# Performance work log

Hardware: AMD Instinct MI355X
Metric: run time of the kernel (lower is better)

## Reference

```python
import jax, jax.numpy as jnp
import numpy as np

N, n, D1, D2 = 16, 1024, 64, 64


def setup_inputs() -> dict:
    key = jax.random.key(0)
    ks = jax.random.split(key, 17)
    f = lambda k, shape: jax.random.normal(k, shape, dtype=jnp.float32)
    return {
        "A": f(ks[0], (N, n, n)),
        "X": f(ks[1], (N, n, D1)),
        "coeffs": f(ks[2], (5,)),
        "wA1": f(ks[3], (1, D1)),
        "wA2": f(ks[4], (1, D1)),
        "w11": f(ks[5], (D2, D1)),
        "w12": f(ks[6], (D2, D1)),
        "w13": f(ks[7], (D2, 1)),
        "w14": f(ks[8], (D2, 1)),
        "w15": f(ks[9], (D2, 1)),
        "w16": f(ks[10], (D2, 1)),
        "w21": f(ks[11], (D2, D1)),
        "w22": f(ks[12], (D2, D1)),
        "w23": f(ks[13], (D2, 1)),
        "w24": f(ks[14], (D2, 1)),
        "w25": f(ks[15], (D2, 1)),
        "w26": f(ks[16], (D2, 1)),
    }


def reference(A, X, coeffs, wA1, wA2, w11, w12, w13, w14, w15, w16,
              w21, w22, w23, w24, w25, w26):
    nn_ = A.shape[-1]
    diag = jnp.diagonal(A, axis1=-2, axis2=-1)          # (N, n)
    mean_diag = diag.mean(-1)                            # (N,)
    rowmean = A.mean(-1)                                 # (N, n) mean over columns
    mean_all = rowmean.mean(-1)                          # (N,)
    mean_X = X.mean(1)                                   # (N, D1)

    p1 = X @ wA1[0]                                      # (N, n)   Linear(D1->1) per node
    p2 = mean_X @ wA2[0]                                 # (N,)     Linear(D1->1) on mean

    # adjacency transform: scalar-weighted A + scalar stats + symmetrized row stats
    A_t = (coeffs[0] * A
           + (coeffs[1] * mean_all + coeffs[2] * mean_diag + p2)[:, None, None]
           + coeffs[3] * (rowmean[:, None, :] + rowmean[:, :, None])
           + coeffs[4] * (diag[:, None, :] + diag[:, :, None])
           + p1[:, None, :] + p1[:, :, None])             # (N, n, n)

    def node_transform(w_x, w_mx, w_col, w_diag, w_mdiag, w_mall):
        per_graph = (mean_X @ w_mx.T                      # (N, D2)
                     + mean_diag[:, None] * w_mdiag[:, 0][None, :]
                     + mean_all[:, None] * w_mall[:, 0][None, :])
        return (jnp.einsum('bnd,ed->bne', X, w_x)         # (N, n, D2)
                + rowmean[:, :, None] * w_col[:, 0]
                + diag[:, :, None] * w_diag[:, 0]
                + per_graph[:, None, :])

    X1_t = node_transform(w11, w12, w13, w14, w15, w16)
    X2_t = node_transform(w21, w22, w23, w24, w25, w26)

    out = A_t @ X2_t / nn_ + X1_t                         # (N, n, D2)
    return (A_t, out)
```

## Files before the change

### kernel.cpp

```cpp
#include <hip/hip_runtime.h>
#include <hip/hip_bf16.h>

#define NGRAPH 16
#define NNODE 1024
#define DDIM 64

typedef __attribute__((ext_vector_type(8))) short bf16x8;
typedef __attribute__((ext_vector_type(4))) float f32x4;

#define OFF_ROWSUM 0
#define OFF_DIAG   16384
#define OFF_P1     32768
#define OFF_R      49152
#define OFF_CS     65536
#define OFF_S      73728
#define OFF_S2P    75840
#define OFF_R2P    92224
#define OFF_BASE0  110656
#define OFF_X2T    1159232

__device__ __forceinline__ unsigned short f2bf(float f) {
    unsigned int u = __float_as_uint(f);
    u = (u + 0x7fffu + ((u >> 16) & 1u)) >> 16;
    return (unsigned short)u;
}

__device__ __forceinline__ unsigned int cvt_pk_bf16(float lo, float hi) {
    unsigned int r;
    asm("v_cvt_pk_bf16_f32 %0, %1, %2" : "=v"(r) : "v"(lo), "v"(hi));
    return r;
}

__device__ __forceinline__ float wave_reduce(float v) {
    #pragma unroll
    for (int off = 32; off; off >>= 1) v += __shfl_down(v, off, 64);
    return v;
}

__global__ __launch_bounds__(256) void kA_stats(const float* __restrict__ A,
                                                const float* __restrict__ X,
                                                const float* __restrict__ wA1,
                                                float* __restrict__ rowsum,
                                                float* __restrict__ diagv,
                                                float* __restrict__ p1,
                                                float* __restrict__ colsum_part) {
    if (blockIdx.x < NGRAPH * NNODE / 4) {
        int row  = blockIdx.x * 4 + (threadIdx.x >> 6);
        int lane = threadIdx.x & 63;
        const float4* b4 = (const float4*)(A + (size_t)row * NNODE);
        float sum = 0.f;
        #pragma unroll
        for (int it = 0; it < 4; ++it) {
            float4 v = b4[lane + it * 64];
            sum += v.x + v.y + v.z + v.w;
        }
        sum = wave_reduce(sum);
        if (lane == 0) {
            rowsum[row] = sum;
            int i = row & (NNODE - 1);
            diagv[row] = ((const float*)b4)[i];
        }
    } else {
        int bid  = blockIdx.x - NGRAPH * NNODE / 4;
        int b    = bid >> 3;
        int blk  = bid & 7;
        int wv   = threadIdx.x >> 6;
        int lane = threadIdx.x & 63;
        float w = wA1[lane];
        float cs = 0.f;
        int row0 = blk * 128 + wv * 32;
        const float* Xb = X + (size_t)b * NNODE * DDIM;
        for (int rI = 0; rI < 32; ++rI) {
            int i = row0 + rI;
            float x = Xb[i * DDIM + lane];
            cs += x;
            float v = wave_reduce(x * w);
            if (lane == 0) p1[b * NNODE + i] = v;
        }
        __shared__ float csl[4][64];
        csl[wv][lane] = cs;
        __syncthreads();
        if (threadIdx.x < 64) {
            float t = csl[0][lane] + csl[1][lane] + csl[2][lane] + csl[3][lane];
            colsum_part[(b * 8 + blk) * 64 + lane] = t;
        }
    }
}

__global__ __launch_bounds__(256) void kB_nodes(const float* __restrict__ X,
                                                const float* __restrict__ coeffs,
                                                const float* __restrict__ wA2,
                                                const float* __restrict__ w11,
                                                const float* __restrict__ w12,
                                                const float* __restrict__ w13,
                                                const float* __restrict__ w14,
                                                const float* __restrict__ w15,
                                                const float* __restrict__ w16,
                                                const float* __restrict__ w21,
                                                const float* __restrict__ w22,
                                                const float* __restrict__ w23,
                                                const float* __restrict__ w24,
                                                const float* __restrict__ w25,
                                                const float* __restrict__ w26,
                                                const float* __restrict__ rowsum,
                                                const float* __restrict__ diagv,
                                                const float* __restrict__ colsum_part,
                                                const float* __restrict__ p1g,
                                                float* __restrict__ rws,
                                                float* __restrict__ base0,
                                                unsigned short* __restrict__ x2tg,
                                                float* __restrict__ S2part,
                                                float* __restrict__ R2part,
                                                float* __restrict__ sArr) {
    __shared__ float Xl[64][68];
    __shared__ float w1l[64][68];
    __shared__ float w2l[64][68];
    __shared__ unsigned short X2Tl[64][68];
    __shared__ float rm_l[64], dg_l[64], r_l[64];
    __shared__ float redS[4][64], redR[4][64];
    __shared__ float redA[4], redD[4];
    __shared__ float mxs[64], p2s;
    __shared__ float pg1_l[64], pg2_l[64];

    int b    = blockIdx.x >> 4;
    int tile = blockIdx.x & 15;
    int i0   = tile * 64;
    int tid  = threadIdx.x;
    int e    = tid & 63;
    int wv   = tid >> 6;

    const float* Xg = X + (size_t)b * (NNODE * DDIM) + (size_t)i0 * DDIM;
    #pragma unroll
    for (int it = 0; it < 4; ++it) {
        int g   = it * 256 + tid;
        int row = g >> 4;
        int c4  = (g & 15) << 2;
        float4 v  = ((const float4*)Xg)[g];
        *(float4*)&Xl[row][c4] = v;
        float4 v1 = ((const float4*)w11)[g];
        *(float4*)&w1l[row][c4] = v1;
        float4 v2 = ((const float4*)w21)[g];
        *(float4*)&w2l[row][c4] = v2;
    }

    float sa = 0.f, sd = 0.f;
    for (int i = tid; i < NNODE; i += 256) {
        sa += rowsum[b * NNODE + i];
        sd += diagv[b * NNODE + i];
    }
    sa = wave_reduce(sa); sd = wave_reduce(sd);
    if (e == 0) { redA[wv] = sa; redD[wv] = sd; }
    if (tid < 64) {
        float mx = 0.f;
        for (int k = 0; k < 8; ++k) mx += colsum_part[(b * 8 + k) * 64 + tid];
        mxs[tid] = mx * (1.f / (float)NNODE);
    }
    __syncthreads();
    float mean_all  = (redA[0] + redA[1] + redA[2] + redA[3]) * (1.f / ((float)NNODE * (float)NNODE));
    float mean_diag = (redD[0] + redD[1] + redD[2] + redD[3]) * (1.f / (float)NNODE);
    float c3 = coeffs[3], c4c = coeffs[4];

    if (wv == 0) {
        float a1 = 0.f;
        for (int d = 0; d < 64; ++d) a1 += mxs[d] * w12[e * 64 + d];
        pg1_l[e] = a1 + mean_diag * w15[e] + mean_all * w16[e];
    } else if (wv == 1) {
        float a2 = 0.f;
        for (int d = 0; d < 64; ++d) a2 += mxs[d] * w22[e * 64 + d];
        pg2_l[e] = a2 + mean_diag * w25[e] + mean_all * w26[e];
    } else if (wv == 2) {
        float v = wave_reduce(mxs[e] * wA2[e]);
        if (e == 0) p2s = v;
    } else {
        float rs  = rowsum[b * NNODE + i0 + e];
        float dgv = diagv[b * NNODE + i0 + e];
        float rmv = rs * (1.f / (float)NNODE);
        rm_l[e] = rmv;
        dg_l[e] = dgv;
        float rv = c3 * rmv + c4c * dgv + p1g[b * NNODE + i0 + e];
        r_l[e] = rv;
        rws[b * NNODE + i0 + e] = rv;
    }
    __syncthreads();
    if (tile == 0 && tid == 0)
        sArr[b] = coeffs[1] * mean_all + coeffs[2] * mean_diag + p2s;

    float w13e = w13[e], w14e = w14[e], w23e = w23[e], w24e = w24[e];
    float pg1e = pg1_l[e], pg2e = pg2_l[e];

    float acc1[16], acc2[16];
    #pragma unroll
    for (int t = 0; t < 16; ++t) { acc1[t] = 0.f; acc2[t] = 0.f; }

    for (int d0 = 0; d0 < 64; d0 += 4) {
        float4 w1v = *(const float4*)&w1l[e][d0];
        float4 w2v = *(const float4*)&w2l[e][d0];
        #pragma unroll
        for (int t = 0; t < 16; ++t) {
            int li = wv + 4 * t;
            float4 xv = *(const float4*)&Xl[li][d0];
            acc1[t] += xv.x * w1v.x + xv.y * w1v.y + xv.z * w1v.z + xv.w * w1v.w;
            acc2[t] += xv.x * w2v.x + xv.y * w2v.y + xv.z * w2v.z + xv.w * w2v.w;
        }
    }

    float s2acc = 0.f, r2acc = 0.f;
    #pragma unroll
    for (int t = 0; t < 16; ++t) {
        int li = wv + 4 * t;
        int i  = i0 + li;
        float rmv = rm_l[li], dgv = dg_l[li];
        float x2t = acc2[t] + rmv * w23e + dgv * w24e + pg2e;
        float b0  = acc1[t] + rmv * w13e + dgv * w14e + pg1e;
        base0[((size_t)(b * NNODE + i)) * 64 + e] = b0;
        X2Tl[e][li] = f2bf(x2t);
        s2acc += x2t;
        r2acc += r_l[li] * x2t;
    }
    redS[wv][e] = s2acc;
    redR[wv][e] = r2acc;
    __syncthreads();

    for (int k = 0; k < 16; ++k) {
        int ep = wv * 16 + k;
        unsigned short v = X2Tl[ep][e];
        x2tg[((size_t)(b * 64 + ep)) * NNODE + i0 + e] = v;
    }
    if (tid < 64) {
        float s2 = redS[0][tid] + redS[1][tid] + redS[2][tid] + redS[3][tid];
        float r2 = redR[0][tid] + redR[1][tid] + redR[2][tid] + redR[3][tid];
        S2part[(b * 16 + tile) * 64 + tid] = s2;
        R2part[(b * 16 + tile) * 64 + tid] = r2;
    }
}

__global__ __launch_bounds__(256) void kC_main(const float* __restrict__ A,
                                               const float* __restrict__ coeffs,
                                               const float* __restrict__ sArr,
                                               const float* __restrict__ rArr,
                                               const unsigned short* __restrict__ x2tg,
                                               const float* __restrict__ base0,
                                               const float* __restrict__ S2part,
                                               const float* __restrict__ R2part,
                                               float* __restrict__ At,
                                               float* __restrict__ outp) {
    __shared__ unsigned short Al[2][16][132];
    __shared__ float r_lds[1024];
    __shared__ float s2_lds[64], r2_lds[64];

    int b    = blockIdx.x >> 6;
    int tile = blockIdx.x & 63;
    int i0   = tile * 16;
    int tid  = threadIdx.x;

    float4 rv = ((const float4*)(rArr + b * NNODE))[tid];
    *(float4*)&r_lds[tid * 4] = rv;
    if (tid < 64) {
        float s2 = 0.f, r2 = 0.f;
        #pragma unroll
        for (int t = 0; t < 16; ++t) {
            s2 += S2part[(b * 16 + t) * 64 + tid];
            r2 += R2part[(b * 16 + t) * 64 + tid];
        }
        s2_lds[tid] = s2 * (1.f / (float)NNODE);
        r2_lds[tid] = r2 * (1.f / (float)NNODE);
    }

    float sb  = sArr[b];
    float c0  = coeffs[0];
    float c0n = c0 * (1.f / (float)NNODE);

    int arow = tid >> 4;
    int acol = (tid & 15) * 8;
    const float* Ab  = A  + ((size_t)(b * NNODE + i0 + arow)) * NNODE + acol;
    float*       Atb = At + ((size_t)(b * NNODE + i0 + arow)) * NNODE + acol;

    int lane = tid & 63, wv = tid >> 6;
    int m = lane & 15, quad = lane >> 4;
    int e = wv * 16 + m;
    const unsigned short* Bg = x2tg + ((size_t)(b * 64 + e)) * NNODE + quad * 8;

    float4 a0 = *(const float4*)(Ab);
    float4 a1 = *(const float4*)(Ab + 4);
    bf16x8 bf0 = *(const bf16x8*)(Bg);
    bf16x8 bf1 = *(const bf16x8*)(Bg + 32);
    bf16x8 bf2 = *(const bf16x8*)(Bg + 64);
    bf16x8 bf3 = *(const bf16x8*)(Bg + 96);

    f32x4 acc = {0.f, 0.f, 0.f, 0.f};

    __syncthreads();

    float bse = sb + r_lds[i0 + arow];

    #pragma unroll
    for (int kt = 0; kt < 8; ++kt) {
        int cidx = kt * 128 + acol;
        float4 rj0 = *(const float4*)&r_lds[cidx];
        float4 rj1 = *(const float4*)&r_lds[cidx + 4];
        f32x4 t0, t1;
        t0.x = fmaf(c0, a0.x, bse + rj0.x);
        t0.y = fmaf(c0, a0.y, bse + rj0.y);
        t0.z = fmaf(c0, a0.z, bse + rj0.z);
        t0.w = fmaf(c0, a0.w, bse + rj0.w);
        t1.x = fmaf(c0, a1.x, bse + rj1.x);
        t1.y = fmaf(c0, a1.y, bse + rj1.y);
        t1.z = fmaf(c0, a1.z, bse + rj1.z);
        t1.w = fmaf(c0, a1.w, bse + rj1.w);
        *(f32x4*)(Atb + kt * 128)     = t0;
        *(f32x4*)(Atb + kt * 128 + 4) = t1;

        uint4 pk;
        pk.x = cvt_pk_bf16(a0.x, a0.y);
        pk.y = cvt_pk_bf16(a0.z, a0.w);
        pk.z = cvt_pk_bf16(a1.x, a1.y);
        pk.w = cvt_pk_bf16(a1.z, a1.w);
        *(uint4*)&Al[kt & 1][arow][acol] = pk;

        bf16x8 n0, n1, n2, n3;
        if (kt < 7) {
            a0 = *(const float4*)(Ab + (kt + 1) * 128);
            a1 = *(const float4*)(Ab + (kt + 1) * 128 + 4);
            n0 = *(const bf16x8*)(Bg + (kt + 1) * 128);
            n1 = *(const bf16x8*)(Bg + (kt + 1) * 128 + 32);
            n2 = *(const bf16x8*)(Bg + (kt + 1) * 128 + 64);
            n3 = *(const bf16x8*)(Bg + (kt + 1) * 128 + 96);
        }

        asm volatile("s_waitcnt lgkmcnt(0)\n\ts_barrier" ::: "memory");

        bf16x8 av0 = *(const bf16x8*)&Al[kt & 1][m][quad * 8];
        bf16x8 av1 = *(const bf16x8*)&Al[kt & 1][m][32 + quad * 8];
        bf16x8 av2 = *(const bf16x8*)&Al[kt & 1][m][64 + quad * 8];
        bf16x8 av3 = *(const bf16x8*)&Al[kt & 1][m][96 + quad * 8];
        acc = __builtin_amdgcn_mfma_f32_16x16x32_bf16(av0, bf0, acc, 0, 0, 0);
        acc = __builtin_amdgcn_mfma_f32_16x16x32_bf16(av1, bf1, acc, 0, 0, 0);
        acc = __builtin_amdgcn_mfma_f32_16x16x32_bf16(av2, bf2, acc, 0, 0, 0);
        acc = __builtin_amdgcn_mfma_f32_16x16x32_bf16(av3, bf3, acc, 0, 0, 0);

        if (kt < 7) { bf0 = n0; bf1 = n1; bf2 = n2; bf3 = n3; }
    }

    float s2 = s2_lds[e];
    float r2 = r2_lds[e];
    #pragma unroll
    for (int reg = 0; reg < 4; ++reg) {
        int i = i0 + quad * 4 + reg;
        float v = acc[reg] * c0n
                + base0[((size_t)(b * NNODE + i)) * 64 + e]
                + (sb + r_lds[i]) * s2 + r2;
        outp[((size_t)(b * NNODE + i)) * 64 + e] = v;
    }
}

extern "C" void kernel_launch(void* const* d_in, const int* in_sizes, int n_in,
                              void* d_out, int out_size, void* d_ws, size_t ws_size,
                              hipStream_t stream) {
    const float* A      = (const float*)d_in[0];
    const float* X      = (const float*)d_in[1];
    const float* coeffs = (const float*)d_in[2];
    const float* wA1    = (const float*)d_in[3];
    const float* wA2    = (const float*)d_in[4];
    const float* w11    = (const float*)d_in[5];
    const float* w12    = (const float*)d_in[6];
    const float* w13    = (const float*)d_in[7];
    const float* w14    = (const float*)d_in[8];
    const float* w15    = (const float*)d_in[9];
    const float* w16    = (const float*)d_in[10];
    const float* w21    = (const float*)d_in[11];
    const float* w22    = (const float*)d_in[12];
    const float* w23    = (const float*)d_in[13];
    const float* w24    = (const float*)d_in[14];
    const float* w25    = (const float*)d_in[15];
    const float* w26    = (const float*)d_in[16];

    float* ws  = (float*)d_ws;
    float* At  = (float*)d_out;
    float* out = (float*)d_out + (size_t)NGRAPH * NNODE * NNODE;

    float* rowsum = ws + OFF_ROWSUM;
    float* diagv  = ws + OFF_DIAG;
    float* p1     = ws + OFF_P1;
    float* rws    = ws + OFF_R;
    float* cspart = ws + OFF_CS;
    float* sArr   = ws + OFF_S;
    float* S2part = ws + OFF_S2P;
    float* R2part = ws + OFF_R2P;
    float* base0  = ws + OFF_BASE0;
    unsigned short* x2tg = (unsigned short*)(ws + OFF_X2T);

    kA_stats<<<NGRAPH * NNODE / 4 + NGRAPH * 8, 256, 0, stream>>>(
        A, X, wA1, rowsum, diagv, p1, cspart);
    kB_nodes<<<NGRAPH * 16, 256, 0, stream>>>(
        X, coeffs, wA2, w11, w12, w13, w14, w15, w16,
        w21, w22, w23, w24, w25, w26,
        rowsum, diagv, cspart, p1,
        rws, base0, x2tg, S2part, R2part, sArr);
    kC_main<<<NGRAPH * 64, 256, 0, stream>>>(
        A, coeffs, sArr, rws, x2tg, base0, S2part, R2part, At, out);
}
```

Measured before the change: 205.3 us.

## Give each wave its own 16-row strip and drop LDS staging of A

Each wave now owns a 16-row strip of A and computes all 64 output columns through four accumulators. The A fragment goes straight from registers into MFMA operands, which removes the LDS staging buffer and the per-iteration barrier. The grid shrinks from 1024 to 256 blocks. In exchange, every wave loads the whole x2t B panel itself instead of sharing it across waves, and the larger register footprint with fewer blocks may reduce the latency hiding available for this streaming kernel.

```diff
diff --git a/kernel.cpp b/kernel.cpp
--- a/kernel.cpp
+++ b/kernel.cpp
@@ -244,14 +244,15 @@
                                                const float* __restrict__ R2part,
                                                float* __restrict__ At,
                                                float* __restrict__ outp) {
-    __shared__ unsigned short Al[2][16][132];
     __shared__ float r_lds[1024];
     __shared__ float s2_lds[64], r2_lds[64];
 
-    int b    = blockIdx.x >> 6;
-    int tile = blockIdx.x & 63;
-    int i0   = tile * 16;
+    int b    = blockIdx.x >> 4;
+    int tb   = blockIdx.x & 15;
     int tid  = threadIdx.x;
+    int lane = tid & 63, wv = tid >> 6;
+    int i0   = (tb * 4 + wv) * 16;
+    int m    = lane & 15, q = lane >> 4;
 
     float4 rv = ((const float4*)(rArr + b * NNODE))[tid];
     *(float4*)&r_lds[tid * 4] = rv;
@@ -270,86 +271,97 @@
     float c0  = coeffs[0];
     float c0n = c0 * (1.f / (float)NNODE);
 
-    int arow = tid >> 4;
-    int acol = (tid & 15) * 8;
-    const float* Ab  = A  + ((size_t)(b * NNODE + i0 + arow)) * NNODE + acol;
-    float*       Atb = At + ((size_t)(b * NNODE + i0 + arow)) * NNODE + acol;
-
-    int lane = tid & 63, wv = tid >> 6;
-    int m = lane & 15, quad = lane >> 4;
-    int e = wv * 16 + m;
-    const unsigned short* Bg = x2tg + ((size_t)(b * 64 + e)) * NNODE + quad * 8;
-
-    float4 a0 = *(const float4*)(Ab);
-    float4 a1 = *(const float4*)(Ab + 4);
-    bf16x8 bf0 = *(const bf16x8*)(Bg);
-    bf16x8 bf1 = *(const bf16x8*)(Bg + 32);
-    bf16x8 bf2 = *(const bf16x8*)(Bg + 64);
-    bf16x8 bf3 = *(const bf16x8*)(Bg + 96);
-
-    f32x4 acc = {0.f, 0.f, 0.f, 0.f};
+    const float* Aw  = A  + ((size_t)(b * NNODE + i0 + m)) * NNODE + q * 8;
+    float*       Atw = At + ((size_t)(b * NNODE + i0 + m)) * NNODE + q * 8;
+    const unsigned short* Bw = x2tg + ((size_t)(b * 64 + m)) * NNODE + q * 8;
+
+    f32x4 a[8], an[8];
+    #pragma unroll
+    for (int ks = 0; ks < 4; ++ks) {
+        a[2 * ks]     = *(const f32x4*)(Aw + ks * 32);
+        a[2 * ks + 1] = *(const f32x4*)(Aw + ks * 32 + 4);
+    }
+
+    f32x4 acc[4];
+    #pragma unroll
+    for (int s = 0; s < 4; ++s) acc[s] = (f32x4){0.f, 0.f, 0.f, 0.f};
 
     __syncthreads();
 
-    float bse = sb + r_lds[i0 + arow];
-
-    #pragma unroll
+    float bse = sb + r_lds[i0 + m];
+
+    #pragma unroll 2
     for (int kt = 0; kt < 8; ++kt) {
-        int cidx = kt * 128 + acol;
-        float4 rj0 = *(const float4*)&r_lds[cidx];
-        float4 rj1 = *(const float4*)&r_lds[cidx + 4];
-        f32x4 t0, t1;
-        t0.x = fmaf(c0, a0.x, bse + rj0.x);
-        t0.y = fmaf(c0, a0.y, bse + rj0.y);
-        t0.z = fmaf(c0, a0.z, bse + rj0.z);
-        t0.w = fmaf(c0, a0.w, bse + rj0.w);
-        t1.x = fmaf(c0, a1.x, bse + rj1.x);
-        t1.y = fmaf(c0, a1.y, bse + rj1.y);
-        t1.z = fmaf(c0, a1.z, bse + rj1.z);
-        t1.w = fmaf(c0, a1.w, bse + rj1.w);
-        *(f32x4*)(Atb + kt * 128)     = t0;
-        *(f32x4*)(Atb + kt * 128 + 4) = t1;
-
-        uint4 pk;
-        pk.x = cvt_pk_bf16(a0.x, a0.y);
-        pk.y = cvt_pk_bf16(a0.z, a0.w);
-        pk.z = cvt_pk_bf16(a1.x, a1.y);
-        pk.w = cvt_pk_bf16(a1.z, a1.w);
-        *(uint4*)&Al[kt & 1][arow][acol] = pk;
-
-        bf16x8 n0, n1, n2, n3;
+        bf16x8 Bf[4][4];
+        #pragma unroll
+        for (int s = 0; s < 4; ++s) {
+            #pragma unroll
+            for (int ks = 0; ks < 4; ++ks) {
+                Bf[s][ks] = *(const bf16x8*)(Bw + (size_t)s * 16 * NNODE + kt * 128 + ks * 32);
+            }
+        }
+
         if (kt < 7) {
-            a0 = *(const float4*)(Ab + (kt + 1) * 128);
-            a1 = *(const float4*)(Ab + (kt + 1) * 128 + 4);
-            n0 = *(const bf16x8*)(Bg + (kt + 1) * 128);
-            n1 = *(const bf16x8*)(Bg + (kt + 1) * 128 + 32);
-            n2 = *(const bf16x8*)(Bg + (kt + 1) * 128 + 64);
-            n3 = *(const bf16x8*)(Bg + (kt + 1) * 128 + 96);
-        }
-
-        asm volatile("s_waitcnt lgkmcnt(0)\n\ts_barrier" ::: "memory");
-
-        bf16x8 av0 = *(const bf16x8*)&Al[kt & 1][m][quad * 8];
-        bf16x8 av1 = *(const bf16x8*)&Al[kt & 1][m][32 + quad * 8];
-        bf16x8 av2 = *(const bf16x8*)&Al[kt & 1][m][64 + quad * 8];
-        bf16x8 av3 = *(const bf16x8*)&Al[kt & 1][m][96 + quad * 8];
-        acc = __builtin_amdgcn_mfma_f32_16x16x32_bf16(av0, bf0, acc, 0, 0, 0);
-        acc = __builtin_amdgcn_mfma_f32_16x16x32_bf16(av1, bf1, acc, 0, 0, 0);
-        acc = __builtin_amdgcn_mfma_f32_16x16x32_bf16(av2, bf2, acc, 0, 0, 0);
-        acc = __builtin_amdgcn_mfma_f32_16x16x32_bf16(av3, bf3, acc, 0, 0, 0);
-
-        if (kt < 7) { bf0 = n0; bf1 = n1; bf2 = n2; bf3 = n3; }
-    }
-
-    float s2 = s2_lds[e];
-    float r2 = r2_lds[e];
-    #pragma unroll
-    for (int reg = 0; reg < 4; ++reg) {
-        int i = i0 + quad * 4 + reg;
-        float v = acc[reg] * c0n
-                + base0[((size_t)(b * NNODE + i)) * 64 + e]
-                + (sb + r_lds[i]) * s2 + r2;
-        outp[((size_t)(b * NNODE + i)) * 64 + e] = v;
+            #pragma unroll
+            for (int ks = 0; ks < 4; ++ks) {
+                an[2 * ks]     = *(const f32x4*)(Aw + (kt + 1) * 128 + ks * 32);
+                an[2 * ks + 1] = *(const f32x4*)(Aw + (kt + 1) * 128 + ks * 32 + 4);
+            }
+        }
+
+        bf16x8 pka[4];
+        #pragma unroll
+        for (int ks = 0; ks < 4; ++ks) {
+            int cb = kt * 128 + ks * 32 + q * 8;
+            f32x4 rj0 = *(const f32x4*)&r_lds[cb];
+            f32x4 rj1 = *(const f32x4*)&r_lds[cb + 4];
+            f32x4 ac0 = a[2 * ks], ac1 = a[2 * ks + 1];
+            f32x4 t0, t1;
+            t0.x = fmaf(c0, ac0.x, bse + rj0.x);
+            t0.y = fmaf(c0, ac0.y, bse + rj0.y);
+            t0.z = fmaf(c0, ac0.z, bse + rj0.z);
+            t0.w = fmaf(c0, ac0.w, bse + rj0.w);
+            t1.x = fmaf(c0, ac1.x, bse + rj1.x);
+            t1.y = fmaf(c0, ac1.y, bse + rj1.y);
+            t1.z = fmaf(c0, ac1.z, bse + rj1.z);
+            t1.w = fmaf(c0, ac1.w, bse + rj1.w);
+            *(f32x4*)(Atw + kt * 128 + ks * 32)     = t0;
+            *(f32x4*)(Atw + kt * 128 + ks * 32 + 4) = t1;
+
+            union { uint4 u; bf16x8 h; } cv;
+            cv.u.x = cvt_pk_bf16(ac0.x, ac0.y);
+            cv.u.y = cvt_pk_bf16(ac0.z, ac0.w);
+            cv.u.z = cvt_pk_bf16(ac1.x, ac1.y);
+            cv.u.w = cvt_pk_bf16(ac1.z, ac1.w);
+            pka[ks] = cv.h;
+        }
+
+        #pragma unroll
+        for (int s = 0; s < 4; ++s) {
+            #pragma unroll
+            for (int ks = 0; ks < 4; ++ks) {
+                acc[s] = __builtin_amdgcn_mfma_f32_16x16x32_bf16(pka[ks], Bf[s][ks], acc[s], 0, 0, 0);
+            }
+        }
+
+        if (kt < 7) {
+            #pragma unroll
+            for (int u = 0; u < 8; ++u) a[u] = an[u];
+        }
+    }
+
+    #pragma unroll
+    for (int s = 0; s < 4; ++s) {
+        float s2 = s2_lds[s * 16 + m];
+        float r2 = r2_lds[s * 16 + m];
+        #pragma unroll
+        for (int reg = 0; reg < 4; ++reg) {
+            int i = i0 + q * 4 + reg;
+            float v = acc[s][reg] * c0n
+                    + base0[((size_t)(b * NNODE + i)) * 64 + s * 16 + m]
+                    + (sb + r_lds[i]) * s2 + r2;
+            outp[((size_t)(b * NNODE + i)) * 64 + s * 16 + m] = v;
+        }
     }
 }
 
@@ -396,6 +408,6 @@
         w21, w22, w23, w24, w25, w26,
         rowsum, diagv, cspart, p1,
         rws, base0, x2tg, S2part, R2part, sArr);
-    kC_main<<<NGRAPH * 64, 256, 0, stream>>>(
+    kC_main<<<NGRAPH * 16, 256, 0, stream>>>(
         A, coeffs, sArr, rws, x2tg, base0, S2part, R2part, At, out);
 }
```

Result: no change. 203.6 us (-0.8%).

## Tile X2T layout per k-block and stage A/B through swizzled LDS buffers

Applied to the files above, without the earlier changes.

The bf16 X2T matrix is now written in k-tile-major blocks of 128 columns, so each k-step's B operand is one contiguous 16KB chunk per graph. The main kernel stages both A (bf16) and B fragments through XOR-swizzled double-buffered LDS, replacing the strided per-lane global reads of B. It also restructures the A loads to full-row float4 coalescing, parallelises the S2/R2 partial reduction across all waves, and sets occupancy hint 3 blocks/CU. The aim is better coalescing and fewer bank conflicts, paid for with more LDS use and extra LDS traffic for B.

```diff
diff --git a/kernel.cpp b/kernel.cpp
--- a/kernel.cpp
+++ b/kernel.cpp
@@ -221,10 +221,12 @@
     redR[wv][e] = r2acc;
     __syncthreads();
 
+    int ktb = tile >> 1;
+    int kof = (tile & 1) << 6;
     for (int k = 0; k < 16; ++k) {
         int ep = wv * 16 + k;
         unsigned short v = X2Tl[ep][e];
-        x2tg[((size_t)(b * 64 + ep)) * NNODE + i0 + e] = v;
+        x2tg[(((size_t)(b * 8 + ktb) * 64 + ep) << 7) + kof + e] = v;
     }
     if (tid < 64) {
         float s2 = redS[0][tid] + redS[1][tid] + redS[2][tid] + redS[3][tid];
@@ -234,7 +236,7 @@
     }
 }
 
-__global__ __launch_bounds__(256) void kC_main(const float* __restrict__ A,
+__global__ __launch_bounds__(256, 3) void kC_main(const float* __restrict__ A,
                                                const float* __restrict__ coeffs,
                                                const float* __restrict__ sArr,
                                                const float* __restrict__ rArr,
@@ -244,112 +246,163 @@
                                                const float* __restrict__ R2part,
                                                float* __restrict__ At,
                                                float* __restrict__ outp) {
-    __shared__ unsigned short Al[2][16][132];
     __shared__ float r_lds[1024];
     __shared__ float s2_lds[64], r2_lds[64];
+    __shared__ float redS[4][64], redR[4][64];
+    __shared__ __align__(16) unsigned char AL[2][4096];
+    __shared__ __align__(16) unsigned char BL[4][2][4096];
 
     int b    = blockIdx.x >> 6;
     int tile = blockIdx.x & 63;
     int i0   = tile * 16;
     int tid  = threadIdx.x;
+    int l    = tid & 63, s = tid >> 6;
+    int m    = l & 15, q = l >> 4;
 
     float4 rv = ((const float4*)(rArr + b * NNODE))[tid];
     *(float4*)&r_lds[tid * 4] = rv;
-    if (tid < 64) {
-        float s2 = 0.f, r2 = 0.f;
+    {
+        float s2p = 0.f, r2p = 0.f;
         #pragma unroll
-        for (int t = 0; t < 16; ++t) {
-            s2 += S2part[(b * 16 + t) * 64 + tid];
-            r2 += R2part[(b * 16 + t) * 64 + tid];
-        }
-        s2_lds[tid] = s2 * (1.f / (float)NNODE);
-        r2_lds[tid] = r2 * (1.f / (float)NNODE);
+        for (int t2 = 0; t2 < 4; ++t2) {
+            int t = s * 4 + t2;
+            s2p += S2part[(b * 16 + t) * 64 + l];
+            r2p += R2part[(b * 16 + t) * 64 + l];
+        }
+        redS[s][l] = s2p;
+        redR[s][l] = r2p;
     }
 
     float sb  = sArr[b];
     float c0  = coeffs[0];
     float c0n = c0 * (1.f / (float)NNODE);
 
-    int arow = tid >> 4;
-    int acol = (tid & 15) * 8;
-    const float* Ab  = A  + ((size_t)(b * NNODE + i0 + arow)) * NNODE + acol;
-    float*       Atb = At + ((size_t)(b * NNODE + i0 + arow)) * NNODE + acol;
-
-    int lane = tid & 63, wv = tid >> 6;
-    int m = lane & 15, quad = lane >> 4;
-    int e = wv * 16 + m;
-    const unsigned short* Bg = x2tg + ((size_t)(b * 64 + e)) * NNODE + quad * 8;
-
-    float4 a0 = *(const float4*)(Ab);
-    float4 a1 = *(const float4*)(Ab + 4);
-    bf16x8 bf0 = *(const bf16x8*)(Bg);
-    bf16x8 bf1 = *(const bf16x8*)(Bg + 32);
-    bf16x8 bf2 = *(const bf16x8*)(Bg + 64);
-    bf16x8 bf3 = *(const bf16x8*)(Bg + 96);
+    int rl0 = 4 * s + (l >> 5);
+    int rl1 = rl0 + 2;
+    const float* A0  = A  + ((size_t)(b * NNODE + i0 + rl0)) * NNODE + (l & 31) * 4;
+    const float* A1  = A0 + 2 * (size_t)NNODE;
+    float*       At0 = At + ((size_t)(b * NNODE + i0 + rl0)) * NNODE + (l & 31) * 4;
+    float*       At1 = At0 + 2 * (size_t)NNODE;
+    const unsigned short* Bg = x2tg + (((size_t)(b * 8) * 64) + 16 * s) * 128 + l * 8;
+
+    unsigned awo0 = rl0 * 256 + (((l & 31) * 8) ^ ((rl0 & 7) << 4));
+    unsigned awo1 = rl1 * 256 + (((l & 31) * 8) ^ ((rl1 & 7) << 4));
+    unsigned bwo[4];
+    #pragma unroll
+    for (int c = 0; c < 4; ++c) {
+        int rp = 4 * c + (l >> 4);
+        bwo[c] = rp * 256 + (((l & 15) * 16) ^ ((rp & 7) << 4));
+    }
+    unsigned fro[4];
+    #pragma unroll
+    for (int ks = 0; ks < 4; ++ks)
+        fro[ks] = m * 256 + ((ks * 64 + q * 16) ^ ((m & 7) << 4));
+
+    f32x4 a0 = *(const f32x4*)(A0);
+    f32x4 a1 = *(const f32x4*)(A1);
+    bf16x8 bb0 = *(const bf16x8*)(Bg);
+    bf16x8 bb1 = *(const bf16x8*)(Bg + 512);
+    bf16x8 bb2 = *(const bf16x8*)(Bg + 1024);
+    bf16x8 bb3 = *(const bf16x8*)(Bg + 1536);
+
+    __syncthreads();
+    if (tid < 64) {
+        s2_lds[tid] = (redS[0][tid] + redS[1][tid] + redS[2][tid] + redS[3][tid]) * (1.f / (float)NNODE);
+        r2_lds[tid] = (redR[0][tid] + redR[1][tid] + redR[2][tid] + redR[3][tid]) * (1.f / (float)NNODE);
+    }
+    float bse0 = sb + r_lds[i0 + rl0];
+    float bse1 = sb + r_lds[i0 + rl1];
+
+    {
+        f32x4 rj = *(const f32x4*)&r_lds[(l & 31) * 4];
+        f32x4 t0, t1;
+        t0.x = fmaf(c0, a0.x, bse0 + rj.x);
+        t0.y = fmaf(c0, a0.y, bse0 + rj.y);
+        t0.z = fmaf(c0, a0.z, bse0 + rj.z);
+        t0.w = fmaf(c0, a0.w, bse0 + rj.w);
+        t1.x = fmaf(c0, a1.x, bse1 + rj.x);
+        t1.y = fmaf(c0, a1.y, bse1 + rj.y);
+        t1.z = fmaf(c0, a1.z, bse1 + rj.z);
+        t1.w = fmaf(c0, a1.w, bse1 + rj.w);
+        *(f32x4*)(At0) = t0;
+        *(f32x4*)(At1) = t1;
+        uint2 w0, w1;
+        w0.x = cvt_pk_bf16(a0.x, a0.y); w0.y = cvt_pk_bf16(a0.z, a0.w);
+        w1.x = cvt_pk_bf16(a1.x, a1.y); w1.y = cvt_pk_bf16(a1.z, a1.w);
+        *(uint2*)(&AL[0][0] + awo0) = w0;
+        *(uint2*)(&AL[0][0] + awo1) = w1;
+        *(bf16x8*)(&BL[s][0][0] + bwo[0]) = bb0;
+        *(bf16x8*)(&BL[s][0][0] + bwo[1]) = bb1;
+        *(bf16x8*)(&BL[s][0][0] + bwo[2]) = bb2;
+        *(bf16x8*)(&BL[s][0][0] + bwo[3]) = bb3;
+    }
+    asm volatile("s_waitcnt lgkmcnt(0)\n\ts_barrier" ::: "memory");
 
     f32x4 acc = {0.f, 0.f, 0.f, 0.f};
 
-    __syncthreads();
-
-    float bse = sb + r_lds[i0 + arow];
-
     #pragma unroll
     for (int kt = 0; kt < 8; ++kt) {
-        int cidx = kt * 128 + acol;
-        float4 rj0 = *(const float4*)&r_lds[cidx];
-        float4 rj1 = *(const float4*)&r_lds[cidx + 4];
-        f32x4 t0, t1;
-        t0.x = fmaf(c0, a0.x, bse + rj0.x);
-        t0.y = fmaf(c0, a0.y, bse + rj0.y);
-        t0.z = fmaf(c0, a0.z, bse + rj0.z);
-        t0.w = fmaf(c0, a0.w, bse + rj0.w);
-        t1.x = fmaf(c0, a1.x, bse + rj1.x);
-        t1.y = fmaf(c0, a1.y, bse + rj1.y);
-        t1.z = fmaf(c0, a1.z, bse + rj1.z);
-        t1.w = fmaf(c0, a1.w, bse + rj1.w);
-        *(f32x4*)(Atb + kt * 128)     = t0;
-        *(f32x4*)(Atb + kt * 128 + 4) = t1;
-
-        uint4 pk;
-        pk.x = cvt_pk_bf16(a0.x, a0.y);
-        pk.y = cvt_pk_bf16(a0.z, a0.w);
-        pk.z = cvt_pk_bf16(a1.x, a1.y);
-        pk.w = cvt_pk_bf16(a1.z, a1.w);
-        *(uint4*)&Al[kt & 1][arow][acol] = pk;
-
-        bf16x8 n0, n1, n2, n3;
+        const int buf = kt & 1, nbuf = buf ^ 1;
+
         if (kt < 7) {
-            a0 = *(const float4*)(Ab + (kt + 1) * 128);
-            a1 = *(const float4*)(Ab + (kt + 1) * 128 + 4);
-            n0 = *(const bf16x8*)(Bg + (kt + 1) * 128);
-            n1 = *(const bf16x8*)(Bg + (kt + 1) * 128 + 32);
-            n2 = *(const bf16x8*)(Bg + (kt + 1) * 128 + 64);
-            n3 = *(const bf16x8*)(Bg + (kt + 1) * 128 + 96);
-        }
-
-        asm volatile("s_waitcnt lgkmcnt(0)\n\ts_barrier" ::: "memory");
-
-        bf16x8 av0 = *(const bf16x8*)&Al[kt & 1][m][quad * 8];
-        bf16x8 av1 = *(const bf16x8*)&Al[kt & 1][m][32 + quad * 8];
-        bf16x8 av2 = *(const bf16x8*)&Al[kt & 1][m][64 + quad * 8];
-        bf16x8 av3 = *(const bf16x8*)&Al[kt & 1][m][96 + quad * 8];
-        acc = __builtin_amdgcn_mfma_f32_16x16x32_bf16(av0, bf0, acc, 0, 0, 0);
-        acc = __builtin_amdgcn_mfma_f32_16x16x32_bf16(av1, bf1, acc, 0, 0, 0);
-        acc = __builtin_amdgcn_mfma_f32_16x16x32_bf16(av2, bf2, acc, 0, 0, 0);
-        acc = __builtin_amdgcn_mfma_f32_16x16x32_bf16(av3, bf3, acc, 0, 0, 0);
-
-        if (kt < 7) { bf0 = n0; bf1 = n1; bf2 = n2; bf3 = n3; }
-    }
-
-    float s2 = s2_lds[e];
-    float r2 = r2_lds[e];
+            a0 = *(const f32x4*)(A0 + (kt + 1) * 128);
+            a1 = *(const f32x4*)(A1 + (kt + 1) * 128);
+            bb0 = *(const bf16x8*)(Bg + (size_t)(kt + 1) * 8192);
+            bb1 = *(const bf16x8*)(Bg + (size_t)(kt + 1) * 8192 + 512);
+            bb2 = *(const bf16x8*)(Bg + (size_t)(kt + 1) * 8192 + 1024);
+            bb3 = *(const bf16x8*)(Bg + (size_t)(kt + 1) * 8192 + 1536);
+        }
+
+        {
+            bf16x8 af0 = *(const bf16x8*)(&AL[buf][0] + fro[0]);
+            bf16x8 bf0 = *(const bf16x8*)(&BL[s][buf][0] + fro[0]);
+            bf16x8 af1 = *(const bf16x8*)(&AL[buf][0] + fro[1]);
+            bf16x8 bf1 = *(const bf16x8*)(&BL[s][buf][0] + fro[1]);
+            bf16x8 af2 = *(const bf16x8*)(&AL[buf][0] + fro[2]);
+            bf16x8 bf2 = *(const bf16x8*)(&BL[s][buf][0] + fro[2]);
+            bf16x8 af3 = *(const bf16x8*)(&AL[buf][0] + fro[3]);
+            bf16x8 bf3 = *(const bf16x8*)(&BL[s][buf][0] + fro[3]);
+            acc = __builtin_amdgcn_mfma_f32_16x16x32_bf16(af0, bf0, acc, 0, 0, 0);
+            acc = __builtin_amdgcn_mfma_f32_16x16x32_bf16(af1, bf1, acc, 0, 0, 0);
+            acc = __builtin_amdgcn_mfma_f32_16x16x32_bf16(af2, bf2, acc, 0, 0, 0);
+            acc = __builtin_amdgcn_mfma_f32_16x16x32_bf16(af3, bf3, acc, 0, 0, 0);
+        }
+
+        if (kt < 7) {
+            f32x4 rj = *(const f32x4*)&r_lds[(kt + 1) * 128 + (l & 31) * 4];
+            f32x4 t0, t1;
+            t0.x = fmaf(c0, a0.x, bse0 + rj.x);
+            t0.y = fmaf(c0, a0.y, bse0 + rj.y);
+            t0.z = fmaf(c0, a0.z, bse0 + rj.z);
+            t0.w = fmaf(c0, a0.w, bse0 + rj.w);
+            t1.x = fmaf(c0, a1.x, bse1 + rj.x);
+            t1.y = fmaf(c0, a1.y, bse1 + rj.y);
+            t1.z = fmaf(c0, a1.z, bse1 + rj.z);
+            t1.w = fmaf(c0, a1.w, bse1 + rj.w);
+            *(f32x4*)(At0 + (kt + 1) * 128) = t0;
+            *(f32x4*)(At1 + (kt + 1) * 128) = t1;
+            uint2 w0, w1;
+            w0.x = cvt_pk_bf16(a0.x, a0.y); w0.y = cvt_pk_bf16(a0.z, a0.w);
+            w1.x = cvt_pk_bf16(a1.x, a1.y); w1.y = cvt_pk_bf16(a1.z, a1.w);
+            *(uint2*)(&AL[nbuf][0] + awo0) = w0;
+            *(uint2*)(&AL[nbuf][0] + awo1) = w1;
+            *(bf16x8*)(&BL[s][nbuf][0] + bwo[0]) = bb0;
+            *(bf16x8*)(&BL[s][nbuf][0] + bwo[1]) = bb1;
+            *(bf16x8*)(&BL[s][nbuf][0] + bwo[2]) = bb2;
+            *(bf16x8*)(&BL[s][nbuf][0] + bwo[3]) = bb3;
+            asm volatile("s_waitcnt lgkmcnt(0)\n\ts_barrier" ::: "memory");
+        }
+    }
+
+    float s2 = s2_lds[16 * s + m];
+    float r2 = r2_lds[16 * s + m];
     #pragma unroll
     for (int reg = 0; reg < 4; ++reg) {
-        int i = i0 + quad * 4 + reg;
+        int i = i0 + q * 4 + reg;
         float v = acc[reg] * c0n
-                + base0[((size_t)(b * NNODE + i)) * 64 + e]
+                + base0[((size_t)(b * NNODE + i)) * 64 + 16 * s + m]
                 + (sb + r_lds[i]) * s2 + r2;
-        outp[((size_t)(b * NNODE + i)) * 64 + e] = v;
+        outp[((size_t)(b * NNODE + i)) * 64 + 16 * s + m] = v;
     }
 }
 
```

Result: faster. 197.8 us (-3.6%).
